# Kernel optimization log

Measured on AMD Instinct MI355X. Metric: run time of the kernel, lower is better.

Reference implementation:

```python
import jax, jax.numpy as jnp
import numpy as np

D_MODEL = 1024
N_HEADS = 16
HEAD_DIM = D_MODEL // N_HEADS


def setup_inputs() -> dict:
    key = jax.random.key(0)
    ks = jax.random.split(key, 5)
    x = jax.random.normal(ks[0], (4, 2048, D_MODEL), dtype=jnp.float32)
    # Linear params (torch Linear: y = x @ W.T + b); store W as [in, out] for einsum.
    s_in = 1.0 / np.sqrt(D_MODEL)
    w_in = jax.random.uniform(ks[1], (D_MODEL, 3 * D_MODEL), jnp.float32, -s_in, s_in)
    b_in = jax.random.uniform(ks[2], (3 * D_MODEL,), jnp.float32, -s_in, s_in)
    w_out = jax.random.uniform(ks[3], (D_MODEL, D_MODEL), jnp.float32, -s_in, s_in)
    b_out = jax.random.uniform(ks[4], (D_MODEL,), jnp.float32, -s_in, s_in)
    return {"x": x, "w_in": w_in, "b_in": b_in, "w_out": w_out, "b_out": b_out}


def reference(x, w_in, b_in, w_out, b_out):
    B, L, D = x.shape
    H, Hd = N_HEADS, HEAD_DIM
    qkv = jnp.einsum('bld,de->ble', x, w_in) + b_in  # [B,L,3D]
    q, k, v = jnp.split(qkv, 3, axis=-1)
    # [B,H,L,Hd]
    q = q.reshape(B, L, H, Hd).transpose(0, 2, 1, 3)
    k = k.reshape(B, L, H, Hd).transpose(0, 2, 1, 3)
    v = v.reshape(B, L, H, Hd).transpose(0, 2, 1, 3)
    scale = 1.0 / np.sqrt(Hd).astype(np.float32)
    scores = jnp.einsum('bhqd,bhkd->bhqk', q, k) * scale  # [B,H,L,L]
    causal = jnp.tril(jnp.ones((L, L), dtype=bool))
    scores = jnp.where(causal, scores, jnp.finfo(scores.dtype).min)
    attn = jax.nn.softmax(scores, axis=-1)
    out = jnp.einsum('bhqk,bhkd->bhqd', attn, v)  # [B,H,L,Hd]
    out = out.transpose(0, 2, 1, 3).reshape(B, L, D)
    return jnp.einsum('bld,de->ble', out, w_out) + b_out
```

## Files before the change

kernel.cpp:

```cpp
#include <hip/hip_runtime.h>

typedef float f32x4 __attribute__((ext_vector_type(4)));
typedef __bf16 bf16x8 __attribute__((ext_vector_type(8)));
typedef short s16x8 __attribute__((ext_vector_type(8)));
typedef int i32x4 __attribute__((ext_vector_type(4)));

__device__ __forceinline__ unsigned short f2bf(float f) {
  union { float f; unsigned u; } v;
  v.f = f;
  unsigned r = v.u + 0x7FFFu + ((v.u >> 16) & 1u);
  return (unsigned short)(r >> 16);
}

__device__ __forceinline__ int cvt_pk_bf16(float lo, float hi) {
  int d;
  asm("v_cvt_pk_bf16_f32 %0, %1, %2" : "=v"(d) : "v"(lo), "v"(hi));
  return d;
}

__device__ __forceinline__ float max3f(float a, float b, float c) {
  float d;
  asm("v_max3_f32 %0, %1, %2, %3" : "=v"(d) : "v"(a), "v"(b), "v"(c));
  return d;
}

#if __has_builtin(__builtin_amdgcn_exp2f)
__device__ __forceinline__ float fexp2(float x) { return __builtin_amdgcn_exp2f(x); }
#else
__device__ __forceinline__ float fexp2(float x) { return exp2f(x); }
#endif

__device__ __forceinline__ void gl_lds16(const void* g, void* l) {
  __builtin_amdgcn_global_load_lds(
      (__attribute__((address_space(1))) void*)g,
      (__attribute__((address_space(3))) void*)l, 16, 0, 0);
}

__global__ __launch_bounds__(256) void k_convert_x(const float* __restrict__ in,
                                                   short* __restrict__ out) {
  int i = (blockIdx.x * 256 + threadIdx.x) * 8;
  const float4* p = (const float4*)(in + i);
  float4 a = p[0], b = p[1];
  s16x8 r;
  r[0] = (short)f2bf(a.x); r[1] = (short)f2bf(a.y);
  r[2] = (short)f2bf(a.z); r[3] = (short)f2bf(a.w);
  r[4] = (short)f2bf(b.x); r[5] = (short)f2bf(b.y);
  r[6] = (short)f2bf(b.z); r[7] = (short)f2bf(b.w);
  *(s16x8*)(out + i) = r;
}

__global__ __launch_bounds__(256) void k_transpose_cvt(const float* __restrict__ in,
                                                       short* __restrict__ out,
                                                       int R, int C) {
  __shared__ short tile[32][33];
  int c0 = blockIdx.x * 32, r0 = blockIdx.y * 32;
  int tx = threadIdx.x, ty = threadIdx.y;
#pragma unroll
  for (int i = 0; i < 32; i += 8)
    tile[ty + i][tx] = (short)f2bf(in[(size_t)(r0 + ty + i) * C + c0 + tx]);
  __syncthreads();
#pragma unroll
  for (int i = 0; i < 32; i += 8)
    out[(size_t)(c0 + ty + i) * R + r0 + tx] = tile[tx][ty + i];
}

__global__ __launch_bounds__(256) void k_qkv_gemm(const short* __restrict__ A,
                                                  const short* __restrict__ B,
                                                  const float* __restrict__ bias,
                                                  short* __restrict__ qb,
                                                  short* __restrict__ kb,
                                                  short* __restrict__ vtb) {
  __shared__ short As[2][128 * 32];
  __shared__ short Bs[2][128 * 32];
  const int tid = threadIdx.x;
  const int lane = tid & 63;
  const int w = tid >> 6;
  const int g = lane >> 4, c = lane & 15;
  const int m0 = blockIdx.y * 128, n0 = blockIdx.x * 128;
  const int wm = (w >> 1) * 64, wn = (w & 1) * 64;
  f32x4 acc[4][4] = {};
  const int p0 = tid, p1 = tid + 256;
  const int rowA0 = p0 >> 2, logA0 = (p0 & 3) ^ ((p0 >> 3) & 3);
  const int rowA1 = p1 >> 2, logA1 = (p1 & 3) ^ ((p1 >> 3) & 3);
  const short* a0 = A + (size_t)(m0 + rowA0) * 1024 + logA0 * 8;
  const short* a1 = A + (size_t)(m0 + rowA1) * 1024 + logA1 * 8;
  const short* b0 = B + (size_t)(n0 + rowA0) * 1024 + logA0 * 8;
  const short* b1 = B + (size_t)(n0 + rowA1) * 1024 + logA1 * 8;

  auto stage = [&](int k0, int buf) {
    gl_lds16(a0 + k0, As[buf] + p0 * 8);
    gl_lds16(a1 + k0, As[buf] + p1 * 8);
    gl_lds16(b0 + k0, Bs[buf] + p0 * 8);
    gl_lds16(b1 + k0, Bs[buf] + p1 * 8);
  };

  stage(0, 0);
  int cur = 0;
  for (int k0 = 0; k0 < 1024; k0 += 32) {
    __syncthreads();
    if (k0 + 32 < 1024) stage(k0 + 32, cur ^ 1);
    const short* as = As[cur];
    const short* bs = Bs[cur];
    bf16x8 af[4], bfr[4];
#pragma unroll
    for (int t = 0; t < 4; t++) {
      int ra = wm + t * 16 + c;
      af[t] = *(const bf16x8*)(as + ra * 32 + (g ^ ((ra >> 1) & 3)) * 8);
      int rb = wn + t * 16 + c;
      bfr[t] = *(const bf16x8*)(bs + rb * 32 + (g ^ ((rb >> 1) & 3)) * 8);
    }
#pragma unroll
    for (int i = 0; i < 4; i++)
#pragma unroll
      for (int jn = 0; jn < 4; jn++)
        acc[i][jn] = __builtin_amdgcn_mfma_f32_16x16x32_bf16(af[i], bfr[jn], acc[i][jn], 0, 0, 0);
    cur ^= 1;
  }

  const int which = n0 >> 10;
  const float qscale = 0.125f * 1.4426950408889634f;
  if (which == 2) {
#pragma unroll
    for (int jn = 0; jn < 4; jn++) {
      const int col = n0 + wn + jn * 16 + c;
      const float bv = bias[col];
      const int cw = col & 1023;
      const int h = cw >> 6, d = cw & 63;
#pragma unroll
      for (int i = 0; i < 4; i++) {
        const int row = m0 + wm + i * 16 + g * 4;
        const int bb = row >> 11, l0 = row & 2047;
        int lo = cvt_pk_bf16(acc[i][jn][0] + bv, acc[i][jn][1] + bv);
        int hi = cvt_pk_bf16(acc[i][jn][2] + bv, acc[i][jn][3] + bv);
        *(int2*)(vtb + (size_t)((bb * 16 + h) * 64 + d) * 2048 + l0) = make_int2(lo, hi);
      }
    }
  } else {
    short* dst = (which == 0) ? qb : kb;
    const float sc = (which == 0) ? qscale : 1.0f;
#pragma unroll
    for (int jn = 0; jn < 4; jn++) {
      const int col = n0 + wn + jn * 16 + c;
      const float bv = bias[col];
      const int cw = col & 1023;
      const int h = cw >> 6, d = cw & 63;
#pragma unroll
      for (int i = 0; i < 4; i++) {
#pragma unroll
        for (int r = 0; r < 4; r++) {
          const int row = m0 + wm + i * 16 + g * 4 + r;
          const int bb = row >> 11, l = row & 2047;
          dst[((size_t)((bb * 16 + h) * 2048 + l) << 6) + d] = (short)f2bf((acc[i][jn][r] + bv) * sc);
        }
      }
    }
  }
}

__device__ __forceinline__ int sigma_row(int rho) {
  return ((rho >> 5) << 5) | (((rho >> 2) & 3) << 3) | (((rho >> 4) & 1) << 2) | (rho & 3);
}

__device__ __forceinline__ void stage_kv512(const short* __restrict__ Kt,
                                            const short* __restrict__ Vtt,
                                            short* ksb, short* vsb, int tid) {
#pragma unroll
  for (int t = 0; t < 2; t++) {
    int p = tid + t * 512;
    int krow = p >> 3, kchk = (p & 7) ^ (krow & 7);
    gl_lds16(Kt + (size_t)sigma_row(krow) * 64 + kchk * 8, ksb + p * 8);
    int dv = p >> 4, vchk = (p & 15) ^ (dv & 15);
    gl_lds16(Vtt + (size_t)dv * 2048 + vchk * 8, vsb + p * 8);
  }
}

__global__ __launch_bounds__(512, 2) void k_attn(const short* __restrict__ Q,
                                                 const short* __restrict__ K,
                                                 const short* __restrict__ Vt,
                                                 short* __restrict__ O) {
  __shared__ short Ks[2][128 * 64];
  __shared__ short Vs[2][64 * 128];
  const int tid = threadIdx.x;
  const int lane = tid & 63;
  const int w = tid >> 6;
  const int quad = lane >> 4, cq = lane & 15;
  const int bh = blockIdx.y;
  const int bb = bh >> 4, h = bh & 15;
  const size_t base = (size_t)bh * (2048 * 64);
  const int pr = blockIdx.x;
  const int qhi = 15 - pr, qlo = pr;
  const int jmax = qhi;
  const int qloc = w * 16 + cq;

  bf16x8 qf[2][2];
#pragma unroll
  for (int mt = 0; mt < 2; mt++) {
    const int qt = mt ? qlo : qhi;
#pragma unroll
    for (int kd = 0; kd < 2; kd++)
      qf[mt][kd] = *(const bf16x8*)(Q + base +
          (size_t)(qt * 128 + w * 16 + cq) * 64 + (kd * 4 + quad) * 8);
  }

  stage_kv512(K + base, Vt + base, Ks[0], Vs[0], tid);

  f32x4 o[2][4] = {};
  float m_run[2] = {-1e30f, -1e30f};
  float l_run[2] = {0.f, 0.f};

  for (int j = 0; j <= jmax; j++) {
    const int cur = j & 1;
    __syncthreads();
    if (j < jmax)
      stage_kv512(K + base + (size_t)(j + 1) * 128 * 64, Vt + base + (j + 1) * 128,
                  Ks[cur ^ 1], Vs[cur ^ 1], tid);
    const short* ks = Ks[cur];
    const short* vs = Vs[cur];
    const bool act1 = (j <= qlo);

    f32x4 s[2][8] = {};
    __builtin_amdgcn_s_setprio(1);
    if (act1) {
#pragma unroll
      for (int kd = 0; kd < 2; kd++)
#pragma unroll
        for (int nt = 0; nt < 8; nt++) {
          int krow = nt * 16 + cq;
          bf16x8 kf = *(const bf16x8*)(ks + krow * 64 + ((kd * 4 + quad) ^ (krow & 7)) * 8);
          s[0][nt] = __builtin_amdgcn_mfma_f32_16x16x32_bf16(kf, qf[0][kd], s[0][nt], 0, 0, 0);
          s[1][nt] = __builtin_amdgcn_mfma_f32_16x16x32_bf16(kf, qf[1][kd], s[1][nt], 0, 0, 0);
        }
    } else {
#pragma unroll
      for (int kd = 0; kd < 2; kd++)
#pragma unroll
        for (int nt = 0; nt < 8; nt++) {
          int krow = nt * 16 + cq;
          bf16x8 kf = *(const bf16x8*)(ks + krow * 64 + ((kd * 4 + quad) ^ (krow & 7)) * 8);
          s[0][nt] = __builtin_amdgcn_mfma_f32_16x16x32_bf16(kf, qf[0][kd], s[0][nt], 0, 0, 0);
        }
    }
    __builtin_amdgcn_s_setprio(0);

    bf16x8 pf[2][4];
    const int nmt = act1 ? 2 : 1;
#pragma unroll
    for (int mt = 0; mt < 2; mt++) {
      if (mt >= nmt) break;
      const bool diag = (j == (mt ? qlo : qhi));
      if (diag) {
#pragma unroll
        for (int nt = 0; nt < 8; nt++)
#pragma unroll
          for (int r = 0; r < 4; r++) {
            int key = (nt >> 1) * 32 + (nt & 1) * 4 + r;
            if (key + quad * 8 > qloc) s[mt][nt][r] = -1e30f;
          }
      }
      float mx;
      {
        float pm[8];
#pragma unroll
        for (int nt = 0; nt < 8; nt++)
          pm[nt] = fmaxf(max3f(s[mt][nt][0], s[mt][nt][1], s[mt][nt][2]), s[mt][nt][3]);
        mx = max3f(max3f(pm[0], pm[1], pm[2]), max3f(pm[3], pm[4], pm[5]),
                   fmaxf(pm[6], pm[7]));
      }
      mx = fmaxf(mx, __shfl_xor(mx, 16));
      mx = fmaxf(mx, __shfl_xor(mx, 32));

      const float mn = fmaxf(m_run[mt], mx);
      const float alpha = fexp2(m_run[mt] - mn);
      m_run[mt] = mn;
      float lt = 0.f;
#pragma unroll
      for (int nt = 0; nt < 8; nt++)
#pragma unroll
        for (int r = 0; r < 4; r++) {
          float p = fexp2(s[mt][nt][r] - mn);
          s[mt][nt][r] = p;
          lt += p;
        }
      l_run[mt] = l_run[mt] * alpha + lt;
#pragma unroll
      for (int dn = 0; dn < 4; dn++) o[mt][dn] *= alpha;
#pragma unroll
      for (int kt = 0; kt < 4; kt++) {
        i32x4 ow;
        ow[0] = cvt_pk_bf16(s[mt][2 * kt][0], s[mt][2 * kt][1]);
        ow[1] = cvt_pk_bf16(s[mt][2 * kt][2], s[mt][2 * kt][3]);
        ow[2] = cvt_pk_bf16(s[mt][2 * kt + 1][0], s[mt][2 * kt + 1][1]);
        ow[3] = cvt_pk_bf16(s[mt][2 * kt + 1][2], s[mt][2 * kt + 1][3]);
        pf[mt][kt] = __builtin_bit_cast(bf16x8, ow);
      }
    }

    __builtin_amdgcn_s_setprio(1);
    if (act1) {
#pragma unroll
      for (int kt = 0; kt < 4; kt++)
#pragma unroll
        for (int dn = 0; dn < 4; dn++) {
          int drow = dn * 16 + cq;
          bf16x8 vtf = *(const bf16x8*)(vs + drow * 128 + ((kt * 4 + quad) ^ (drow & 15)) * 8);
          o[0][dn] = __builtin_amdgcn_mfma_f32_16x16x32_bf16(vtf, pf[0][kt], o[0][dn], 0, 0, 0);
          o[1][dn] = __builtin_amdgcn_mfma_f32_16x16x32_bf16(vtf, pf[1][kt], o[1][dn], 0, 0, 0);
        }
    } else {
#pragma unroll
      for (int kt = 0; kt < 4; kt++)
#pragma unroll
        for (int dn = 0; dn < 4; dn++) {
          int drow = dn * 16 + cq;
          bf16x8 vtf = *(const bf16x8*)(vs + drow * 128 + ((kt * 4 + quad) ^ (drow & 15)) * 8);
          o[0][dn] = __builtin_amdgcn_mfma_f32_16x16x32_bf16(vtf, pf[0][kt], o[0][dn], 0, 0, 0);
        }
    }
    __builtin_amdgcn_s_setprio(0);
  }

#pragma unroll
  for (int mt = 0; mt < 2; mt++) {
    const int qt = mt ? qlo : qhi;
    float lf = l_run[mt];
    lf += __shfl_xor(lf, 16);
    lf += __shfl_xor(lf, 32);
    const float inv = 1.f / lf;
    const size_t rb = ((size_t)(bb * 2048 + qt * 128 + w * 16 + cq)) * 1024 + h * 64;
#pragma unroll
    for (int dn = 0; dn < 4; dn++) {
      int d0 = cvt_pk_bf16(o[mt][dn][0] * inv, o[mt][dn][1] * inv);
      int d1 = cvt_pk_bf16(o[mt][dn][2] * inv, o[mt][dn][3] * inv);
      *(int2*)(O + rb + dn * 16 + quad * 4) = make_int2(d0, d1);
    }
  }
}

__global__ __launch_bounds__(256) void k_out_gemm(const short* __restrict__ A,
                                                  const short* __restrict__ B,
                                                  const float* __restrict__ bias,
                                                  float* __restrict__ out) {
  __shared__ short As[2][128 * 32];
  __shared__ short Bs[2][128 * 32];
  const int tid = threadIdx.x;
  const int lane = tid & 63;
  const int w = tid >> 6;
  const int g = lane >> 4, c = lane & 15;
  const int m0 = blockIdx.y * 128, n0 = blockIdx.x * 128;
  const int wm = (w >> 1) * 64, wn = (w & 1) * 64;
  f32x4 acc[4][4] = {};
  const int p0 = tid, p1 = tid + 256;
  const int rowA0 = p0 >> 2, logA0 = (p0 & 3) ^ ((p0 >> 3) & 3);
  const int rowA1 = p1 >> 2, logA1 = (p1 & 3) ^ ((p1 >> 3) & 3);
  const short* a0 = A + (size_t)(m0 + rowA0) * 1024 + logA0 * 8;
  const short* a1 = A + (size_t)(m0 + rowA1) * 1024 + logA1 * 8;
  const short* b0 = B + (size_t)(n0 + rowA0) * 1024 + logA0 * 8;
  const short* b1 = B + (size_t)(n0 + rowA1) * 1024 + logA1 * 8;

  auto stage = [&](int k0, int buf) {
    gl_lds16(a0 + k0, As[buf] + p0 * 8);
    gl_lds16(a1 + k0, As[buf] + p1 * 8);
    gl_lds16(b0 + k0, Bs[buf] + p0 * 8);
    gl_lds16(b1 + k0, Bs[buf] + p1 * 8);
  };

  stage(0, 0);
  int cur = 0;
  for (int k0 = 0; k0 < 1024; k0 += 32) {
    __syncthreads();
    if (k0 + 32 < 1024) stage(k0 + 32, cur ^ 1);
    const short* as = As[cur];
    const short* bs = Bs[cur];
    bf16x8 af[4], bfr[4];
#pragma unroll
    for (int t = 0; t < 4; t++) {
      int ra = wm + t * 16 + c;
      af[t] = *(const bf16x8*)(as + ra * 32 + (g ^ ((ra >> 1) & 3)) * 8);
      int rb = wn + t * 16 + c;
      bfr[t] = *(const bf16x8*)(bs + rb * 32 + (g ^ ((rb >> 1) & 3)) * 8);
    }
#pragma unroll
    for (int i = 0; i < 4; i++)
#pragma unroll
      for (int jn = 0; jn < 4; jn++)
        acc[i][jn] = __builtin_amdgcn_mfma_f32_16x16x32_bf16(af[i], bfr[jn], acc[i][jn], 0, 0, 0);
    cur ^= 1;
  }
#pragma unroll
  for (int jn = 0; jn < 4; jn++) {
    const int col = n0 + wn + jn * 16 + c;
    const float bv = bias[col];
#pragma unroll
    for (int i = 0; i < 4; i++) {
#pragma unroll
      for (int r = 0; r < 4; r++) {
        const int row = m0 + wm + i * 16 + g * 4 + r;
        out[(size_t)row * 1024 + col] = acc[i][jn][r] + bv;
      }
    }
  }
}

extern "C" void kernel_launch(void* const* d_in, const int* in_sizes, int n_in,
                              void* d_out, int out_size, void* d_ws, size_t ws_size,
                              hipStream_t stream) {
  const float* x     = (const float*)d_in[0];
  const float* w_in  = (const float*)d_in[1];
  const float* b_in  = (const float*)d_in[2];
  const float* w_out = (const float*)d_in[3];
  const float* b_out = (const float*)d_in[4];
  float* out = (float*)d_out;
  char* ws = (char*)d_ws;
  short* x_bf   = (short*)(ws);
  short* w_inT  = (short*)(ws + (16ull << 20));
  short* w_outT = (short*)(ws + (22ull << 20));
  short* qb     = (short*)(ws + (24ull << 20));
  short* kb     = (short*)(ws + (40ull << 20));
  short* vtb    = (short*)(ws + (56ull << 20));
  short* ao     = (short*)(ws + (72ull << 20));

  k_convert_x<<<dim3(4096), dim3(256), 0, stream>>>(x, x_bf);
  k_transpose_cvt<<<dim3(96, 32), dim3(32, 8), 0, stream>>>(w_in, w_inT, 1024, 3072);
  k_transpose_cvt<<<dim3(32, 32), dim3(32, 8), 0, stream>>>(w_out, w_outT, 1024, 1024);
  k_qkv_gemm<<<dim3(24, 64), dim3(256), 0, stream>>>(x_bf, w_inT, b_in, qb, kb, vtb);
  k_attn<<<dim3(8, 64), dim3(512), 0, stream>>>(qb, kb, vtb, ao);
  k_out_gemm<<<dim3(8, 64), dim3(256), 0, stream>>>(ao, w_outT, b_out, out);
}
```

Baseline: 280.9 us.

## Rewrite QKV GEMM with 256x256 tiles, 4-stage LDS pipeline and block swizzle

The QKV projection GEMM moves from 128x128 tiles with 256 threads and double buffering to 256x256 tiles with 512 threads. A four-stage LDS ring with explicit vmcnt waits, split A/B staging across two phases, s_setprio around the MFMA bursts and a grid remap that groups neighbouring tiles for L2 reuse are meant to hide global latency and raise arithmetic intensity. The output GEMM is switched to a single-buffered load-sync-compute-sync loop, which lowers LDS use but exposes load latency. Register pressure from 32 accumulators per thread and the 128KB LDS footprint may limit occupancy.

```diff
diff --git a/kernel.cpp b/kernel.cpp
--- a/kernel.cpp
+++ b/kernel.cpp
@@ -64,93 +64,136 @@
     out[(size_t)(c0 + ty + i) * R + r0 + tx] = tile[tx][ty + i];
 }
 
-__global__ __launch_bounds__(256) void k_qkv_gemm(const short* __restrict__ A,
-                                                  const short* __restrict__ B,
-                                                  const float* __restrict__ bias,
-                                                  short* __restrict__ qb,
-                                                  short* __restrict__ kb,
-                                                  short* __restrict__ vtb) {
-  __shared__ short As[2][128 * 32];
-  __shared__ short Bs[2][128 * 32];
+#define QKV_PHASE(J, MH, STGA, STGB, STJ, WVM)                                \
+  {                                                                           \
+    const short* as_ = SA[(J) & 3];                                           \
+    bf16x8 afr[4];                                                            \
+    _Pragma("unroll")                                                         \
+    for (int m_ = 0; m_ < 4; m_++)                                            \
+      afr[m_] = *(const bf16x8*)(as_ + aoff + ((MH)*4 + m_) * 512);           \
+    if (MH == 0) {                                                            \
+      const short* bs_ = SB[(J) & 3];                                         \
+      _Pragma("unroll")                                                       \
+      for (int n_ = 0; n_ < 4; n_++)                                          \
+        bfrag[n_] = *(const bf16x8*)(bs_ + boff + n_ * 512);                  \
+    }                                                                         \
+    if (STGA) {                                                               \
+      const int kb_ = (STJ)*32;                                               \
+      short* d_ = SA[(STJ)&3];                                                \
+      gl_lds16(Abase + kb_, d_ + tid * 8);                                    \
+      gl_lds16(Abase + kb_ + (size_t)128 * 1024, d_ + (512 + tid) * 8);       \
+    }                                                                         \
+    if (STGB) {                                                               \
+      const int kb_ = (STJ)*32;                                               \
+      short* d_ = SB[(STJ)&3];                                                \
+      gl_lds16(Bbase + kb_, d_ + tid * 8);                                    \
+      gl_lds16(Bbase + kb_ + (size_t)128 * 1024, d_ + (512 + tid) * 8);       \
+    }                                                                         \
+    __builtin_amdgcn_s_barrier();                                             \
+    asm volatile("s_waitcnt lgkmcnt(0)" ::: "memory");                        \
+    __builtin_amdgcn_s_setprio(1);                                            \
+    _Pragma("unroll")                                                         \
+    for (int m_ = 0; m_ < 4; m_++)                                            \
+      _Pragma("unroll")                                                       \
+      for (int n_ = 0; n_ < 4; n_++)                                          \
+        acc[(MH)*4 + m_][n_] = __builtin_amdgcn_mfma_f32_16x16x32_bf16(       \
+            afr[m_], bfrag[n_], acc[(MH)*4 + m_][n_], 0, 0, 0);               \
+    __builtin_amdgcn_s_setprio(0);                                            \
+    if (WVM == 8) asm volatile("s_waitcnt vmcnt(8)" ::: "memory");            \
+    if (WVM == 4) asm volatile("s_waitcnt vmcnt(4)" ::: "memory");            \
+    if (WVM == 0) asm volatile("s_waitcnt vmcnt(0)" ::: "memory");            \
+    __builtin_amdgcn_s_barrier();                                             \
+  }
+
+__global__ __launch_bounds__(512, 2) void k_qkv_gemm(const short* __restrict__ A,
+                                                     const short* __restrict__ B,
+                                                     const float* __restrict__ bias,
+                                                     short* __restrict__ qb,
+                                                     short* __restrict__ kb,
+                                                     short* __restrict__ vtb) {
+  __shared__ short SA[4][256 * 32];
+  __shared__ short SB[4][256 * 32];
   const int tid = threadIdx.x;
   const int lane = tid & 63;
+  const int quad = lane >> 4, cq = lane & 15;
   const int w = tid >> 6;
-  const int g = lane >> 4, c = lane & 15;
-  const int m0 = blockIdx.y * 128, n0 = blockIdx.x * 128;
-  const int wm = (w >> 1) * 64, wn = (w & 1) * 64;
-  f32x4 acc[4][4] = {};
-  const int p0 = tid, p1 = tid + 256;
-  const int rowA0 = p0 >> 2, logA0 = (p0 & 3) ^ ((p0 >> 3) & 3);
-  const int rowA1 = p1 >> 2, logA1 = (p1 & 3) ^ ((p1 >> 3) & 3);
-  const short* a0 = A + (size_t)(m0 + rowA0) * 1024 + logA0 * 8;
-  const short* a1 = A + (size_t)(m0 + rowA1) * 1024 + logA1 * 8;
-  const short* b0 = B + (size_t)(n0 + rowA0) * 1024 + logA0 * 8;
-  const short* b1 = B + (size_t)(n0 + rowA1) * 1024 + logA1 * 8;
-
-  auto stage = [&](int k0, int buf) {
-    gl_lds16(a0 + k0, As[buf] + p0 * 8);
-    gl_lds16(a1 + k0, As[buf] + p1 * 8);
-    gl_lds16(b0 + k0, Bs[buf] + p0 * 8);
-    gl_lds16(b1 + k0, Bs[buf] + p1 * 8);
-  };
-
-  stage(0, 0);
-  int cur = 0;
-  for (int k0 = 0; k0 < 1024; k0 += 32) {
-    __syncthreads();
-    if (k0 + 32 < 1024) stage(k0 + 32, cur ^ 1);
-    const short* as = As[cur];
-    const short* bs = Bs[cur];
-    bf16x8 af[4], bfr[4];
-#pragma unroll
-    for (int t = 0; t < 4; t++) {
-      int ra = wm + t * 16 + c;
-      af[t] = *(const bf16x8*)(as + ra * 32 + (g ^ ((ra >> 1) & 3)) * 8);
-      int rb = wn + t * 16 + c;
-      bfr[t] = *(const bf16x8*)(bs + rb * 32 + (g ^ ((rb >> 1) & 3)) * 8);
-    }
-#pragma unroll
-    for (int i = 0; i < 4; i++)
-#pragma unroll
-      for (int jn = 0; jn < 4; jn++)
-        acc[i][jn] = __builtin_amdgcn_mfma_f32_16x16x32_bf16(af[i], bfr[jn], acc[i][jn], 0, 0, 0);
-    cur ^= 1;
-  }
+  const int wmi = w >> 2, wni = w & 3;
+
+  const int orig = blockIdx.y * 12 + blockIdx.x;
+  const int wg = (orig & 7) * 48 + (orig >> 3);
+  const int bn = wg % 12, bm = wg / 12;
+  const int m0 = bm * 256, n0 = bn * 256;
+
+  const int srow = tid >> 2;
+  const int sg = (tid & 3) ^ ((tid >> 3) & 3);
+  const short* Abase = A + (size_t)(m0 + srow) * 1024 + sg * 8;
+  const short* Bbase = B + (size_t)(n0 + srow) * 1024 + sg * 8;
+
+  const int xchk = (quad ^ ((cq >> 1) & 3)) * 8;
+  const int aoff = (wmi * 128 + cq) * 32 + xchk;
+  const int boff = (wni * 64 + cq) * 32 + xchk;
+
+  f32x4 acc[8][4] = {};
+  bf16x8 bfrag[4];
+
+  {
+#pragma unroll
+    for (int j = 0; j < 3; j++) {
+      const int kb_ = j * 32;
+      gl_lds16(Abase + kb_, SA[j] + tid * 8);
+      gl_lds16(Abase + kb_ + (size_t)128 * 1024, SA[j] + (512 + tid) * 8);
+      gl_lds16(Bbase + kb_, SB[j] + tid * 8);
+      gl_lds16(Bbase + kb_ + (size_t)128 * 1024, SB[j] + (512 + tid) * 8);
+    }
+  }
+  asm volatile("s_waitcnt vmcnt(8)" ::: "memory");
+  __builtin_amdgcn_s_barrier();
+
+  for (int j = 0; j < 29; ++j) {
+    QKV_PHASE(j, 0, 1, 0, j + 3, -1);
+    QKV_PHASE(j, 1, 0, 1, j + 3, 8);
+  }
+  QKV_PHASE(29, 0, 0, 0, 0, -1);
+  QKV_PHASE(29, 1, 0, 0, 0, 4);
+  QKV_PHASE(30, 0, 0, 0, 0, -1);
+  QKV_PHASE(30, 1, 0, 0, 0, 0);
+  QKV_PHASE(31, 0, 0, 0, 0, -1);
+  QKV_PHASE(31, 1, 0, 0, 0, -1);
 
   const int which = n0 >> 10;
   const float qscale = 0.125f * 1.4426950408889634f;
   if (which == 2) {
 #pragma unroll
-    for (int jn = 0; jn < 4; jn++) {
-      const int col = n0 + wn + jn * 16 + c;
+    for (int fn = 0; fn < 4; fn++) {
+      const int col = n0 + wni * 64 + fn * 16 + cq;
       const float bv = bias[col];
       const int cw = col & 1023;
       const int h = cw >> 6, d = cw & 63;
 #pragma unroll
-      for (int i = 0; i < 4; i++) {
-        const int row = m0 + wm + i * 16 + g * 4;
-        const int bb = row >> 11, l0 = row & 2047;
-        int lo = cvt_pk_bf16(acc[i][jn][0] + bv, acc[i][jn][1] + bv);
-        int hi = cvt_pk_bf16(acc[i][jn][2] + bv, acc[i][jn][3] + bv);
-        *(int2*)(vtb + (size_t)((bb * 16 + h) * 64 + d) * 2048 + l0) = make_int2(lo, hi);
+      for (int fm = 0; fm < 8; fm++) {
+        const int row = m0 + wmi * 128 + fm * 16 + quad * 4;
+        const int bb2 = row >> 11, l0 = row & 2047;
+        int lo = cvt_pk_bf16(acc[fm][fn][0] + bv, acc[fm][fn][1] + bv);
+        int hi = cvt_pk_bf16(acc[fm][fn][2] + bv, acc[fm][fn][3] + bv);
+        *(int2*)(vtb + (size_t)((bb2 * 16 + h) * 64 + d) * 2048 + l0) = make_int2(lo, hi);
       }
     }
   } else {
     short* dst = (which == 0) ? qb : kb;
     const float sc = (which == 0) ? qscale : 1.0f;
 #pragma unroll
-    for (int jn = 0; jn < 4; jn++) {
-      const int col = n0 + wn + jn * 16 + c;
+    for (int fn = 0; fn < 4; fn++) {
+      const int col = n0 + wni * 64 + fn * 16 + cq;
       const float bv = bias[col];
       const int cw = col & 1023;
       const int h = cw >> 6, d = cw & 63;
 #pragma unroll
-      for (int i = 0; i < 4; i++) {
+      for (int fm = 0; fm < 8; fm++) {
 #pragma unroll
         for (int r = 0; r < 4; r++) {
-          const int row = m0 + wm + i * 16 + g * 4 + r;
-          const int bb = row >> 11, l = row & 2047;
-          dst[((size_t)((bb * 16 + h) * 2048 + l) << 6) + d] = (short)f2bf((acc[i][jn][r] + bv) * sc);
+          const int row = m0 + wmi * 128 + fm * 16 + quad * 4 + r;
+          const int bb2 = row >> 11, l = row & 2047;
+          dst[((size_t)((bb2 * 16 + h) * 2048 + l) << 6) + d] = (short)f2bf((acc[fm][fn][r] + bv) * sc);
         }
       }
     }
@@ -340,8 +383,8 @@
                                                   const short* __restrict__ B,
                                                   const float* __restrict__ bias,
                                                   float* __restrict__ out) {
-  __shared__ short As[2][128 * 32];
-  __shared__ short Bs[2][128 * 32];
+  __shared__ short As[128 * 32];
+  __shared__ short Bs[128 * 32];
   const int tid = threadIdx.x;
   const int lane = tid & 63;
   const int w = tid >> 6;
@@ -356,35 +399,29 @@
   const short* a1 = A + (size_t)(m0 + rowA1) * 1024 + logA1 * 8;
   const short* b0 = B + (size_t)(n0 + rowA0) * 1024 + logA0 * 8;
   const short* b1 = B + (size_t)(n0 + rowA1) * 1024 + logA1 * 8;
-
-  auto stage = [&](int k0, int buf) {
-    gl_lds16(a0 + k0, As[buf] + p0 * 8);
-    gl_lds16(a1 + k0, As[buf] + p1 * 8);
-    gl_lds16(b0 + k0, Bs[buf] + p0 * 8);
-    gl_lds16(b1 + k0, Bs[buf] + p1 * 8);
-  };
-
-  stage(0, 0);
-  int cur = 0;
+  short* lA0 = As + p0 * 8; short* lA1 = As + p1 * 8;
+  short* lB0 = Bs + p0 * 8; short* lB1 = Bs + p1 * 8;
+
   for (int k0 = 0; k0 < 1024; k0 += 32) {
+    gl_lds16(a0 + k0, lA0);
+    gl_lds16(a1 + k0, lA1);
+    gl_lds16(b0 + k0, lB0);
+    gl_lds16(b1 + k0, lB1);
     __syncthreads();
-    if (k0 + 32 < 1024) stage(k0 + 32, cur ^ 1);
-    const short* as = As[cur];
-    const short* bs = Bs[cur];
     bf16x8 af[4], bfr[4];
 #pragma unroll
     for (int t = 0; t < 4; t++) {
       int ra = wm + t * 16 + c;
-      af[t] = *(const bf16x8*)(as + ra * 32 + (g ^ ((ra >> 1) & 3)) * 8);
+      af[t] = *(const bf16x8*)(As + ra * 32 + (g ^ ((ra >> 1) & 3)) * 8);
       int rb = wn + t * 16 + c;
-      bfr[t] = *(const bf16x8*)(bs + rb * 32 + (g ^ ((rb >> 1) & 3)) * 8);
+      bfr[t] = *(const bf16x8*)(Bs + rb * 32 + (g ^ ((rb >> 1) & 3)) * 8);
     }
 #pragma unroll
     for (int i = 0; i < 4; i++)
 #pragma unroll
       for (int jn = 0; jn < 4; jn++)
         acc[i][jn] = __builtin_amdgcn_mfma_f32_16x16x32_bf16(af[i], bfr[jn], acc[i][jn], 0, 0, 0);
-    cur ^= 1;
+    __syncthreads();
   }
 #pragma unroll
   for (int jn = 0; jn < 4; jn++) {
@@ -422,7 +459,7 @@
   k_convert_x<<<dim3(4096), dim3(256), 0, stream>>>(x, x_bf);
   k_transpose_cvt<<<dim3(96, 32), dim3(32, 8), 0, stream>>>(w_in, w_inT, 1024, 3072);
   k_transpose_cvt<<<dim3(32, 32), dim3(32, 8), 0, stream>>>(w_out, w_outT, 1024, 1024);
-  k_qkv_gemm<<<dim3(24, 64), dim3(256), 0, stream>>>(x_bf, w_inT, b_in, qb, kb, vtb);
+  k_qkv_gemm<<<dim3(12, 32), dim3(512), 0, stream>>>(x_bf, w_inT, b_in, qb, kb, vtb);
   k_attn<<<dim3(8, 64), dim3(512), 0, stream>>>(qb, kb, vtb, ao);
   k_out_gemm<<<dim3(8, 64), dim3(256), 0, stream>>>(ao, w_outT, b_out, out);
 }
```

Result: slower. 287.0 us (+2.2%).
